# Performance work log

Hardware: AMD Instinct MI355X
Metric: run time of the kernel (lower is better)

The kernel has to match this reference:

```python
import jax, jax.numpy as jnp
import numpy as np
from jax import lax

EPS = 1e-5

def binarize_ste(x):
    # sign binarization to {-1,+1} (0 -> +1) with straight-through gradient
    s = jnp.where(x >= 0, 1.0, -1.0).astype(x.dtype)
    return x + lax.stop_gradient(s - x)

def bn(x, gamma, beta, mean, var):
    # inference-mode batchnorm; broadcast over channel axis 1 for 4D, axis 1 for 2D
    if x.ndim == 4:
        shape = (1, -1, 1, 1)
    else:
        shape = (1, -1)
    inv = gamma.reshape(shape) / jnp.sqrt(var.reshape(shape) + EPS)
    return (x - mean.reshape(shape)) * inv + beta.reshape(shape)

def conv_rep(x, w):
    # replicate (edge) padding of 1, then valid 3x3 conv, NCHW/OIHW
    xp = jnp.pad(x, ((0, 0), (0, 0), (1, 1), (1, 1)), mode='edge')
    return lax.conv_general_dilated(xp, binarize_ste(w), (1, 1), 'VALID',
                                    dimension_numbers=('NCHW', 'OIHW', 'NCHW'))

def maxpool2(x):
    return lax.reduce_window(x, -jnp.inf, lax.max, (1, 1, 2, 2), (1, 1, 2, 2), 'VALID')

def hardtanh(x):
    return jnp.clip(x, -1.0, 1.0)

def setup_inputs() -> dict:
    key = jax.random.key(0)
    ks = jax.random.split(key, 16)
    B = 2048
    inp = {
        'x': jax.random.normal(ks[0], (B, 1, 28, 28), jnp.float32),
        'conv1_w': jax.random.normal(ks[1], (64, 1, 3, 3), jnp.float32),
        'bn1_gamma': jax.random.uniform(ks[2], (64,), jnp.float32),
        'bn1_beta': jax.random.normal(ks[3], (64,), jnp.float32),
        'bn1_mean': jax.random.normal(ks[4], (64,), jnp.float32),
        'bn1_var': jax.random.uniform(ks[5], (64,), jnp.float32),
        'conv2_w': jax.random.normal(ks[6], (64, 64, 3, 3), jnp.float32),
        'bn2_gamma': jax.random.uniform(ks[7], (64,), jnp.float32),
        'bn2_beta': jax.random.normal(ks[8], (64,), jnp.float32),
        'bn2_mean': jax.random.normal(ks[9], (64,), jnp.float32),
        'bn2_var': jax.random.uniform(ks[10], (64,), jnp.float32),
        'fc1_w': jax.random.normal(ks[11], (2048, 3136), jnp.float32),
        'bn3_gamma': jax.random.uniform(ks[12], (2048,), jnp.float32),
        'bn3_beta': jax.random.normal(ks[13], (2048,), jnp.float32),
        'bn3_mean': jax.random.normal(ks[14], (2048,), jnp.float32),
        'bn3_var': jax.random.uniform(ks[15], (2048,), jnp.float32),
        'fc2_w': jax.random.normal(jax.random.fold_in(key, 99), (10, 2048), jnp.float32),
        'scale': jnp.array([0.001], jnp.float32),
    }
    return inp

def reference(x, conv1_w, bn1_gamma, bn1_beta, bn1_mean, bn1_var,
              conv2_w, bn2_gamma, bn2_beta, bn2_mean, bn2_var,
              fc1_w, bn3_gamma, bn3_beta, bn3_mean, bn3_var,
              fc2_w, scale):
    # block 1: binarized conv -> BN -> hardtanh -> binarize -> maxpool
    h = conv_rep(x, conv1_w)                          # [B,64,28,28]
    h = binarize_ste(hardtanh(bn(h, bn1_gamma, bn1_beta, bn1_mean, bn1_var)))
    h = maxpool2(h)                                   # [B,64,14,14]
    # block 2
    h = conv_rep(h, conv2_w)                          # [B,64,14,14]
    h = binarize_ste(hardtanh(bn(h, bn2_gamma, bn2_beta, bn2_mean, bn2_var)))
    h = maxpool2(h)                                   # [B,64,7,7]
    h = h.reshape(h.shape[0], -1)                     # [B,3136] (C*H*W order)
    # fc block
    h = h @ binarize_ste(fc1_w).T                     # [B,2048]
    h = binarize_ste(hardtanh(bn(h, bn3_gamma, bn3_beta, bn3_mean, bn3_var)))
    h = h @ binarize_ste(fc2_w).T                     # [B,10]
    return h * scale
```

## Files before the change

### kernel.cpp

```cpp
#include <hip/hip_runtime.h>
#include <cstdint>

#define EPS 1e-5f

typedef unsigned long long u64;
typedef unsigned int u32;
typedef unsigned short u16;
typedef unsigned char u8;
typedef float v2f __attribute__((ext_vector_type(2)));

__device__ __forceinline__ int clampi(int v, int lo, int hi) {
    return v < lo ? lo : (v > hi ? hi : v);
}

__device__ __forceinline__ v2f v2_fma(v2f a, v2f b, v2f c) {
#if __has_builtin(__builtin_elementwise_fma)
    return __builtin_elementwise_fma(a, b, c);
#else
    v2f r; r.x = __builtin_fmaf(a.x, b.x, c.x); r.y = __builtin_fmaf(a.y, b.y, c.y); return r;
#endif
}
__device__ __forceinline__ v2f v2_min(v2f a, v2f b) {
#if __has_builtin(__builtin_elementwise_min)
    return __builtin_elementwise_min(a, b);
#else
    v2f r; r.x = fminf(a.x, b.x); r.y = fminf(a.y, b.y); return r;
#endif
}
__device__ __forceinline__ v2f v2_max(v2f a, v2f b) {
#if __has_builtin(__builtin_elementwise_max)
    return __builtin_elementwise_max(a, b);
#else
    v2f r; r.x = fmaxf(a.x, b.x); r.y = fmaxf(a.y, b.y); return r;
#endif
}


__global__ __launch_bounds__(256) void prep_all(
    const float* __restrict__ fc1_w, u64* __restrict__ wp,
    const float* __restrict__ conv1_w, const float* __restrict__ conv2_w,
    const float* __restrict__ fc2_w,
    const float* __restrict__ g1, const float* __restrict__ b1,
    const float* __restrict__ m1, const float* __restrict__ v1,
    const float* __restrict__ g2, const float* __restrict__ b2,
    const float* __restrict__ m2, const float* __restrict__ v2,
    v2f* __restrict__ s1d, u64* __restrict__ w2p, u64* __restrict__ w2pk,
    float4* __restrict__ bnc1, float4* __restrict__ bnc2)
{
    __shared__ float ls[3136];
    int bid = blockIdx.x;
    if (bid < 2048) {
        int o = bid;
        const float4* row4 = (const float4*)(fc1_w + o * 3136);
        for (int i = threadIdx.x; i < 784; i += 256)
            ((float4*)ls)[i] = row4[i];
        __syncthreads();
        int p = threadIdx.x;
        if (p < 49) {
            u64 word = 0;
            #pragma unroll
            for (int c = 0; c < 64; c++)
                word |= (u64)(ls[c * 49 + p] >= 0.f) << c;
            wp[p * 2048 + o] = word;
        }
    } else {
        int t = (bid - 2048) * 256 + threadIdx.x;
        if (t < 576) {
            float s = (conv1_w[t] >= 0.f) ? 1.f : -1.f;
            v2f d; d.x = s; d.y = s;
            s1d[t] = d;
        } else if (t < 1152) {
            int u = t - 576;
            int co = u / 9, tap = u % 9;
            u64 word = 0;
            for (int ci = 0; ci < 64; ci++)
                word |= (u64)(conv2_w[(co * 64 + ci) * 9 + tap] >= 0.f) << ci;
            w2p[u] = word;
        } else if (t < 1472) {
            int u = t - 1152;
            int o = u / 32, k = u % 32;
            u64 word = 0;
            for (int j = 0; j < 64; j++)
                word |= (u64)(fc2_w[o * 2048 + k * 64 + j] >= 0.f) << j;
            w2pk[u] = word;
        } else if (t < 1536) {
            int ch = t - 1472;
            bnc1[ch] = make_float4(m1[ch], g1[ch] / sqrtf(v1[ch] + EPS), b1[ch], 0.f);
        } else if (t < 1600) {
            int ch = t - 1536;
            bnc2[ch] = make_float4(m2[ch], g2[ch] / sqrtf(v2[ch] + EPS), b2[ch], 0.f);
        }
    }
}


__global__ __launch_bounds__(256) void k_conv1(
    const float* __restrict__ x, const v2f* __restrict__ s1d,
    const float4* __restrict__ bnc1, u64* __restrict__ out1)
{
    int tid = threadIdx.x;
    int g = blockIdx.y;
    int base = g * 16;

    int idx = blockIdx.x * 256 + tid;
    int b = idx / 196, p = idx % 196;
    int pi = p / 14, pj = p % 14;

    const float* xb = x + b * 784;
    int rr[4], cc[4];
    #pragma unroll
    for (int r = 0; r < 4; r++) rr[r] = clampi(2 * pi - 1 + r, 0, 27) * 28;
    #pragma unroll
    for (int c = 0; c < 4; c++) cc[c] = clampi(2 * pj - 1 + c, 0, 27);
    float patch[4][4];
    #pragma unroll
    for (int r = 0; r < 4; r++)
        #pragma unroll
        for (int c = 0; c < 4; c++)
            patch[r][c] = xb[rr[r] + cc[c]];

    v2f pp[4][3];
    #pragma unroll
    for (int r = 0; r < 4; r++)
        #pragma unroll
        for (int j = 0; j < 3; j++) {
            v2f t; t.x = patch[r][j]; t.y = patch[r][j + 1];
            pp[r][j] = t;
        }

    u32 word = 0;
    #pragma unroll 4
    for (int ch = 0; ch < 16; ch++) {
        const v2f* w = s1d + (base + ch) * 9;
        v2f a01 = 0.f, a23 = 0.f;
        #pragma unroll
        for (int ki = 0; ki < 3; ki++)
            #pragma unroll
            for (int kj = 0; kj < 3; kj++) {
                v2f ww = w[ki * 3 + kj];
                a01 = v2_fma(pp[ki][kj],     ww, a01);
                a23 = v2_fma(pp[ki + 1][kj], ww, a23);
            }
        v2f mn = v2_min(a01, a23);
        v2f mx = v2_max(a01, a23);
        float vmin = fminf(mn.x, mn.y);
        float vmax = fmaxf(mx.x, mx.y);
        float4 c4 = bnc1[base + ch];
        int bit = (((vmin - c4.x) * c4.y + c4.z) >= 0.f) |
                  (((vmax - c4.x) * c4.y + c4.z) >= 0.f);
        word |= (u32)bit << ch;
    }
    ((u16*)out1)[idx * 4 + g] = (u16)word;
}


__global__ __launch_bounds__(256) void k_conv2(
    const u64* __restrict__ in, const u64* __restrict__ w2p,
    const float4* __restrict__ bnc2, u64* __restrict__ out2)
{
    int tid = threadIdx.x;
    int g = blockIdx.y;
    int base = g * 8;

    int idx = blockIdx.x * 256 + tid;
    int b = idx / 49, p = idx % 49;
    int pi = p / 7, pj = p % 7;

    const u64* ib = in + b * 196;
    int rr[4], cc[4];
    #pragma unroll
    for (int r = 0; r < 4; r++) rr[r] = clampi(2 * pi - 1 + r, 0, 13) * 14;
    #pragma unroll
    for (int c = 0; c < 4; c++) cc[c] = clampi(2 * pj - 1 + c, 0, 13);
    u64 a[4][4];
    #pragma unroll
    for (int r = 0; r < 4; r++)
        #pragma unroll
        for (int c = 0; c < 4; c++)
            a[r][c] = ib[rr[r] + cc[c]];

    u32 word = 0;
    #pragma unroll
    for (int co = 0; co < 8; co++) {
        const u64* w = w2p + (base + co) * 9;
        int s00 = 0, s01 = 0, s10 = 0, s11 = 0;
        #pragma unroll
        for (int ki = 0; ki < 3; ki++)
            #pragma unroll
            for (int kj = 0; kj < 3; kj++) {
                u64 ww = w[ki * 3 + kj];
                s00 += __popcll(a[ki][kj] ^ ww);
                s01 += __popcll(a[ki][kj + 1] ^ ww);
                s10 += __popcll(a[ki + 1][kj] ^ ww);
                s11 += __popcll(a[ki + 1][kj + 1] ^ ww);
            }
        int smin = min(min(s00, s01), min(s10, s11));
        int smax = max(max(s00, s01), max(s10, s11));
        float4 c4 = bnc2[base + co];
        int bit = (((float)(576 - 2 * smin) - c4.x) * c4.y + c4.z >= 0.f) |
                  (((float)(576 - 2 * smax) - c4.x) * c4.y + c4.z >= 0.f);
        word |= (u32)bit << co;
    }
    ((u8*)out2)[idx * 8 + g] = (u8)word;
}


#define NB 8

__global__ __launch_bounds__(256) void k_fc1(
    const u64* __restrict__ act, const u64* __restrict__ wp,
    const float* __restrict__ g, const float* __restrict__ bt,
    const float* __restrict__ mn, const float* __restrict__ vr,
    u64* __restrict__ out3)
{
    int tid = threadIdx.x;
    int btile = blockIdx.x >> 3;
    int otile = blockIdx.x & 7;
    int b0 = btile * NB;
    int o = otile * 256 + tid;
    const u64* ab = act + b0 * 49;

    int sums[NB];
    #pragma unroll
    for (int i = 0; i < NB; i++) sums[i] = 0;

    for (int p = 0; p < 49; p++) {
        u64 w = wp[p * 2048 + o];
        #pragma unroll
        for (int bb = 0; bb < NB; bb++)
            sums[bb] += __popcll(ab[bb * 49 + p] ^ w);
    }

    float iv = g[o] / sqrtf(vr[o] + EPS);
    float m = mn[o], be = bt[o];
    #pragma unroll
    for (int bb = 0; bb < NB; bb++) {
        float y = ((float)(3136 - 2 * sums[bb]) - m) * iv + be;
        u64 ball = __ballot(y >= 0.f);
        if ((tid & 63) == 0) out3[(b0 + bb) * 32 + (o >> 6)] = ball;
    }
}


__global__ void k_fc2(const u64* __restrict__ act, const u64* __restrict__ w2,
                      const float* __restrict__ scale, float* __restrict__ out)
{
    int idx = blockIdx.x * 256 + threadIdx.x;
    if (idx >= 2048 * 16) return;
    int b = idx >> 4, o = idx & 15;
    if (o >= 10) return;
    int s = 0;
    #pragma unroll
    for (int k = 0; k < 32; k++)
        s += __popcll(act[b * 32 + k] ^ w2[o * 32 + k]);
    out[b * 10 + o] = scale[0] * (float)(2048 - 2 * s);
}


extern "C" void kernel_launch(void* const* d_in, const int* in_sizes, int n_in,
                              void* d_out, int out_size, void* d_ws, size_t ws_size,
                              hipStream_t stream) {
    const float* x        = (const float*)d_in[0];
    const float* conv1_w  = (const float*)d_in[1];
    const float* bn1_g    = (const float*)d_in[2];
    const float* bn1_b    = (const float*)d_in[3];
    const float* bn1_m    = (const float*)d_in[4];
    const float* bn1_v    = (const float*)d_in[5];
    const float* conv2_w  = (const float*)d_in[6];
    const float* bn2_g    = (const float*)d_in[7];
    const float* bn2_b    = (const float*)d_in[8];
    const float* bn2_m    = (const float*)d_in[9];
    const float* bn2_v    = (const float*)d_in[10];
    const float* fc1_w    = (const float*)d_in[11];
    const float* bn3_g    = (const float*)d_in[12];
    const float* bn3_b    = (const float*)d_in[13];
    const float* bn3_m    = (const float*)d_in[14];
    const float* bn3_v    = (const float*)d_in[15];
    const float* fc2_w    = (const float*)d_in[16];
    const float* scale    = (const float*)d_in[17];
    float* out = (float*)d_out;

    char* ws = (char*)d_ws;
    v2f*    s1d  = (v2f*)   (ws + 0);
    u64*    w2p  = (u64*)   (ws + 4608);
    float4* bnc1 = (float4*)(ws + 9216);
    float4* bnc2 = (float4*)(ws + 10240);
    u64*    w2pk = (u64*)   (ws + 11264);
    u64*    wp   = (u64*)   (ws + 16384);
    u64*    out1 = (u64*)   (ws + 819200);
    u64*    out2 = (u64*)   (ws + 4030464);
    u64*    out3 = (u64*)   (ws + 4833280);

    hipLaunchKernelGGL(prep_all, dim3(2055), dim3(256), 0, stream,
                       fc1_w, wp, conv1_w, conv2_w, fc2_w,
                       bn1_g, bn1_b, bn1_m, bn1_v,
                       bn2_g, bn2_b, bn2_m, bn2_v,
                       s1d, w2p, w2pk, bnc1, bnc2);

    hipLaunchKernelGGL(k_conv1, dim3(1568, 4), dim3(256), 0, stream,
                       x, s1d, bnc1, out1);
    hipLaunchKernelGGL(k_conv2, dim3(392, 8), dim3(256), 0, stream,
                       out1, w2p, bnc2, out2);
    hipLaunchKernelGGL(k_fc1, dim3(2048), dim3(256), 0, stream,
                       out2, wp, bn3_g, bn3_b, bn3_m, bn3_v, out3);
    hipLaunchKernelGGL(k_fc2, dim3(128), dim3(256), 0, stream,
                       out3, w2pk, scale, out);
}
```

Measured before the change: 205.1 us.

## Fuse fc1 weight packing into conv1 launch and pack bits via wave ballot

The fc1 weight bit-packing moves out of the prep kernel and into the conv1 kernel as an extra 2048 blocks. This lets the large memory-bound packing run alongside conv1 compute, and the prep kernel shrinks to 7 blocks of tiny setup work. The packing itself now uses a 64-lane __ballot per output word instead of one thread looping over 64 LDS reads, which spreads the work across all four waves. The cost is a shared-memory allocation in the conv1 blocks, which may lower their occupancy, and a mixed-workload grid whose block scheduling is less uniform.

```diff
diff --git a/kernel.cpp b/kernel.cpp
--- a/kernel.cpp
+++ b/kernel.cpp
@@ -36,8 +36,7 @@
 }
 
 
-__global__ __launch_bounds__(256) void prep_all(
-    const float* __restrict__ fc1_w, u64* __restrict__ wp,
+__global__ __launch_bounds__(256) void prep_tiny(
     const float* __restrict__ conv1_w, const float* __restrict__ conv2_w,
     const float* __restrict__ fc2_w,
     const float* __restrict__ g1, const float* __restrict__ b1,
@@ -47,62 +46,63 @@
     v2f* __restrict__ s1d, u64* __restrict__ w2p, u64* __restrict__ w2pk,
     float4* __restrict__ bnc1, float4* __restrict__ bnc2)
 {
+    int t = blockIdx.x * 256 + threadIdx.x;
+    if (t < 576) {
+        float s = (conv1_w[t] >= 0.f) ? 1.f : -1.f;
+        v2f d; d.x = s; d.y = s;
+        s1d[t] = d;
+    } else if (t < 1152) {
+        int u = t - 576;
+        int co = u / 9, tap = u % 9;
+        u64 word = 0;
+        for (int ci = 0; ci < 64; ci++)
+            word |= (u64)(conv2_w[(co * 64 + ci) * 9 + tap] >= 0.f) << ci;
+        w2p[u] = word;
+    } else if (t < 1472) {
+        int u = t - 1152;
+        int o = u / 32, k = u % 32;
+        u64 word = 0;
+        for (int j = 0; j < 64; j++)
+            word |= (u64)(fc2_w[o * 2048 + k * 64 + j] >= 0.f) << j;
+        w2pk[u] = word;
+    } else if (t < 1536) {
+        int ch = t - 1472;
+        bnc1[ch] = make_float4(m1[ch], g1[ch] / sqrtf(v1[ch] + EPS), b1[ch], 0.f);
+    } else if (t < 1600) {
+        int ch = t - 1536;
+        bnc2[ch] = make_float4(m2[ch], g2[ch] / sqrtf(v2[ch] + EPS), b2[ch], 0.f);
+    }
+}
+
+
+__global__ __launch_bounds__(256) void k_conv1r(
+    const float* __restrict__ x, const v2f* __restrict__ s1d,
+    const float4* __restrict__ bnc1, u64* __restrict__ out1,
+    const float* __restrict__ fc1_w, u64* __restrict__ wp)
+{
     __shared__ float ls[3136];
+    int tid = threadIdx.x;
     int bid = blockIdx.x;
+
     if (bid < 2048) {
         int o = bid;
         const float4* row4 = (const float4*)(fc1_w + o * 3136);
-        for (int i = threadIdx.x; i < 784; i += 256)
+        for (int i = tid; i < 784; i += 256)
             ((float4*)ls)[i] = row4[i];
         __syncthreads();
-        int p = threadIdx.x;
-        if (p < 49) {
-            u64 word = 0;
-            #pragma unroll
-            for (int c = 0; c < 64; c++)
-                word |= (u64)(ls[c * 49 + p] >= 0.f) << c;
-            wp[p * 2048 + o] = word;
+        int lane = tid & 63, wv = tid >> 6;
+        for (int p = wv; p < 49; p += 4) {
+            float v = ls[lane * 49 + p];
+            u64 ball = __ballot(v >= 0.f);
+            if (lane == 0) wp[p * 2048 + o] = ball;
         }
-    } else {
-        int t = (bid - 2048) * 256 + threadIdx.x;
-        if (t < 576) {
-            float s = (conv1_w[t] >= 0.f) ? 1.f : -1.f;
-            v2f d; d.x = s; d.y = s;
-            s1d[t] = d;
-        } else if (t < 1152) {
-            int u = t - 576;
-            int co = u / 9, tap = u % 9;
-            u64 word = 0;
-            for (int ci = 0; ci < 64; ci++)
-                word |= (u64)(conv2_w[(co * 64 + ci) * 9 + tap] >= 0.f) << ci;
-            w2p[u] = word;
-        } else if (t < 1472) {
-            int u = t - 1152;
-            int o = u / 32, k = u % 32;
-            u64 word = 0;
-            for (int j = 0; j < 64; j++)
-                word |= (u64)(fc2_w[o * 2048 + k * 64 + j] >= 0.f) << j;
-            w2pk[u] = word;
-        } else if (t < 1536) {
-            int ch = t - 1472;
-            bnc1[ch] = make_float4(m1[ch], g1[ch] / sqrtf(v1[ch] + EPS), b1[ch], 0.f);
-        } else if (t < 1600) {
-            int ch = t - 1536;
-            bnc2[ch] = make_float4(m2[ch], g2[ch] / sqrtf(v2[ch] + EPS), b2[ch], 0.f);
-        }
-    }
-}
-
-
-__global__ __launch_bounds__(256) void k_conv1(
-    const float* __restrict__ x, const v2f* __restrict__ s1d,
-    const float4* __restrict__ bnc1, u64* __restrict__ out1)
-{
-    int tid = threadIdx.x;
-    int g = blockIdx.y;
+        return;
+    }
+
+    int idx2 = bid - 2048;
+    int g = idx2 & 3;
     int base = g * 16;
-
-    int idx = blockIdx.x * 256 + tid;
+    int idx = (idx2 >> 2) * 256 + tid;
     int b = idx / 196, p = idx % 196;
     int pi = p / 14, pj = p % 14;
 
@@ -291,14 +291,14 @@
     u64*    out2 = (u64*)   (ws + 4030464);
     u64*    out3 = (u64*)   (ws + 4833280);
 
-    hipLaunchKernelGGL(prep_all, dim3(2055), dim3(256), 0, stream,
-                       fc1_w, wp, conv1_w, conv2_w, fc2_w,
+    hipLaunchKernelGGL(prep_tiny, dim3(7), dim3(256), 0, stream,
+                       conv1_w, conv2_w, fc2_w,
                        bn1_g, bn1_b, bn1_m, bn1_v,
                        bn2_g, bn2_b, bn2_m, bn2_v,
                        s1d, w2p, w2pk, bnc1, bnc2);
 
-    hipLaunchKernelGGL(k_conv1, dim3(1568, 4), dim3(256), 0, stream,
-                       x, s1d, bnc1, out1);
+    hipLaunchKernelGGL(k_conv1r, dim3(2048 + 6272), dim3(256), 0, stream,
+                       x, s1d, bnc1, out1, fc1_w, wp);
     hipLaunchKernelGGL(k_conv2, dim3(392, 8), dim3(256), 0, stream,
                        out1, w2p, bnc2, out2);
     hipLaunchKernelGGL(k_fc1, dim3(2048), dim3(256), 0, stream,
```

Result: no change. 205.6 us (+0.3%).
